# Kernel optimization log

Hardware: AMD Instinct MI355X
Metric: run time of the kernel (lower is better)

## Reference

```python
import jax, jax.numpy as jnp
import numpy as np

B, S, H, R = 2, 4096, 2048, 2048
NB, CW = 16, 4
BW = R // NB


def _block_diag_linear(x, w, b):
    # x: [B,S,R]; w: [NB,BW,BW]; b: [NB,BW]
    xb = x.reshape(x.shape[0], x.shape[1], NB, BW)
    out = jnp.einsum('bsni,nij->bsnj', xb, w) + b
    return out.reshape(x.shape)


def _causal_conv1d(x, conv_w, conv_b):
    # depthwise causal temporal conv: out[t] = sum_i w[i]*x[t-CW+1+i] + b
    xp = jnp.pad(x, ((0, 0), (CW - 1, 0), (0, 0)))
    out = conv_b
    for i in range(CW):
        out = out + conv_w[i] * xp[:, i:i + x.shape[1], :]
    return out


def _rg_lru_scan(x, x_gate_pre, a_gate_pre, a_param):
    gate_x = jax.nn.sigmoid(x_gate_pre)
    gate_a = jax.nn.sigmoid(a_gate_pre)
    log_a = -8.0 * gate_a * jax.nn.softplus(a_param)  # [B,S,R]
    a = jnp.exp(log_a)
    multiplier = jnp.sqrt(-jnp.expm1(2.0 * log_a))  # sqrt(1 - a^2)
    norm_x = x * gate_x * multiplier
    # h_t = a_t * h_{t-1} + norm_x_t via parallel associative scan over time
    def combine(c1, c2):
        a1, b1 = c1
        a2, b2 = c2
        return a1 * a2, a2 * b1 + b2
    _, h = jax.lax.associative_scan(combine, (a, norm_x), axis=1)
    return h


def setup_inputs() -> dict:
    key = jax.random.key(0)
    ks = jax.random.split(key, 9)
    x = jax.random.normal(ks[0], (B, S, H), dtype=jnp.float32)
    W_xy = jax.random.normal(ks[1], (2 * R, H), dtype=jnp.float32) / np.sqrt(H)
    ig_w = jax.random.normal(ks[2], (NB, BW, BW), dtype=jnp.float32) / np.sqrt(BW)
    ig_b = jnp.zeros((NB, BW), dtype=jnp.float32)
    ag_w = jax.random.normal(ks[3], (NB, BW, BW), dtype=jnp.float32) / np.sqrt(BW)
    ag_b = jnp.zeros((NB, BW), dtype=jnp.float32)
    # forget_init: a = a_real in [0.9, 0.999]; a_param = softplus^{-1}(-log(a_real))
    unif = jax.random.uniform(ks[4], (R,), dtype=jnp.float32)
    a_real = 0.5 * jnp.log(unif * (0.999 ** 2 - 0.9 ** 2) + 0.9 ** 2 + 1e-8)
    a_param = jnp.log(jnp.expm1(-a_real))
    conv_w = jax.random.normal(ks[5], (CW, R), dtype=jnp.float32) / np.sqrt(CW * R)
    conv_b = jnp.zeros((R,), dtype=jnp.float32)
    # resid_proj is zero-init in the module; use small random so output is non-trivial
    W_resid = 0.02 * jax.random.normal(ks[6], (H, R), dtype=jnp.float32)
    return {"x": x, "W_xy": W_xy, "ig_w": ig_w, "ig_b": ig_b,
            "ag_w": ag_w, "ag_b": ag_b, "a_param": a_param,
            "conv_w": conv_w, "conv_b": conv_b, "W_resid": W_resid}


def reference(x, W_xy, ig_w, ig_b, ag_w, ag_b, a_param, conv_w, conv_b, W_resid):
    xy = jnp.einsum('bsh,rh->bsr', x, W_xy)  # [B,S,2R]
    xr, y = jnp.split(xy, 2, axis=-1)
    xc = _causal_conv1d(xr, conv_w, conv_b)
    x_gate_pre = _block_diag_linear(xc, ig_w, ig_b)
    a_gate_pre = _block_diag_linear(xc, ag_w, ag_b)
    h = _rg_lru_scan(xc, x_gate_pre, a_gate_pre, a_param)
    out = jnp.einsum('bsr,hr->bsh', jax.nn.gelu(y, approximate=False) * h, W_resid)
    return out
```

## Files before the change

kernel.cpp:

```cpp
#include <hip/hip_runtime.h>
#include <hip/hip_bf16.h>

typedef __hip_bfloat16 bf16;
typedef __attribute__((ext_vector_type(8))) short s16x8;
typedef __attribute__((ext_vector_type(4))) float f32x4;

#define B_ 2
#define S_ 4096
#define H_ 2048
#define R_ 2048
#define M_ 8192
#define NB_ 16
#define BW_ 128
#define CHUNK 64
#define NCH 64

__device__ __forceinline__ short f2b_s(float f) {
    return (short)__builtin_bit_cast(unsigned short, __float2bfloat16(f));
}
__device__ __forceinline__ float b2f_s(short s) {
    unsigned int u = ((unsigned int)(unsigned short)s) << 16;
    return __builtin_bit_cast(float, u);
}
__device__ __forceinline__ float sigm_fast(float x) { return 1.f / (1.f + __expf(-x)); }

__device__ __forceinline__ void async_g2l(const void* g, void* l) {
    __builtin_amdgcn_global_load_lds((const __attribute__((address_space(1))) void*)g,
                                     (__attribute__((address_space(3))) void*)l, 16, 0, 0);
}

__global__ __launch_bounds__(256) void cast_all(const float* __restrict__ x,
                                                const float* __restrict__ wxy,
                                                const float* __restrict__ wres,
                                                bf16* __restrict__ xbf,
                                                bf16* __restrict__ wxyb,
                                                bf16* __restrict__ wresb) {
    int idx = blockIdx.x * 256 + threadIdx.x;
    const float* in; bf16* out; int off;
    if (idx < 2097152)      { in = x;    out = xbf;   off = idx; }
    else if (idx < 3145728) { in = wxy;  out = wxyb;  off = idx - 2097152; }
    else                    { in = wres; out = wresb; off = idx - 3145728; }
    size_t i8 = (size_t)off * 8;
    float4 v0 = *(const float4*)(in + i8);
    float4 v1 = *(const float4*)(in + i8 + 4);
    s16x8 o;
    o[0] = f2b_s(v0.x); o[1] = f2b_s(v0.y); o[2] = f2b_s(v0.z); o[3] = f2b_s(v0.w);
    o[4] = f2b_s(v1.x); o[5] = f2b_s(v1.y); o[6] = f2b_s(v1.z); o[7] = f2b_s(v1.w);
    *(s16x8*)(out + i8) = o;
}

__global__ __launch_bounds__(256) void wcast_T(const float* __restrict__ igw,
                                               const float* __restrict__ agw,
                                               const float* __restrict__ apar,
                                               bf16* __restrict__ wT,
                                               float* __restrict__ sp8) {
    int blk = blockIdx.x;
    int tid = threadIdx.x;
    if (blk == 32) {
#pragma unroll
        for (int it = 0; it < 8; ++it) {
            int r = it * 256 + tid;
            float ap = apar[r];
            sp8[r] = 8.f * (ap > 20.f ? ap : log1pf(expf(ap)));
        }
        return;
    }
    __shared__ float tile[128 * 129];
    int p = blk >> 4, n = blk & 15;
    const float* w = (p ? agw : igw) + (size_t)n * 16384;
#pragma unroll
    for (int it = 0; it < 64; ++it) {
        int u = it * 256 + tid;
        tile[(u >> 7) * 129 + (u & 127)] = w[u];
    }
    __syncthreads();
    bf16* o = wT + (size_t)blk * 16384;
#pragma unroll
    for (int it = 0; it < 64; ++it) {
        int u = it * 256 + tid;
        o[u] = __float2bfloat16(tile[(u & 127) * 129 + (u >> 7)]);
    }
}

__device__ __forceinline__ void store_c(float* p, float v) { *p = v; }
__device__ __forceinline__ void store_c(bf16* p, float v) { *p = __float2bfloat16(v); }

template <typename OutT>
__global__ __launch_bounds__(256, 4) void gemm_bt(const bf16* __restrict__ A,
                                                  const bf16* __restrict__ Bm,
                                                  OutT* __restrict__ C,
                                                  int K, int lda, int ldb, int ldc) {
    __shared__ __align__(16) short As[128 * 64];
    __shared__ __align__(16) short Bs[128 * 64];
    const int tid = threadIdx.x;
    const int lane = tid & 63, wave = tid >> 6;
    const int waveM = wave >> 1, waveN = wave & 1;
    const int mBase = blockIdx.y * 128, nBase = blockIdx.x * 128;
    const int fm = lane & 15, q = lane >> 4;

    f32x4 acc[4][4];
#pragma unroll
    for (int i = 0; i < 4; ++i)
#pragma unroll
        for (int j = 0; j < 4; ++j) acc[i][j] = (f32x4){0.f, 0.f, 0.f, 0.f};

    for (int k0 = 0; k0 < K; k0 += 64) {
        __syncthreads();
#pragma unroll
        for (int it = 0; it < 4; ++it) {
            int off = it * 4096 + tid * 16;
            int r = off >> 7;
            int g = ((off & 127) >> 4) ^ (r & 7);
            async_g2l(A + (size_t)(mBase + r) * lda + k0 + g * 8, (char*)As + off);
            async_g2l(Bm + (size_t)(nBase + r) * ldb + k0 + g * 8, (char*)Bs + off);
        }
        __syncthreads();
#pragma unroll
        for (int s = 0; s < 2; ++s) {
            s16x8 af[4], bfr[4];
#pragma unroll
            for (int i = 0; i < 4; ++i) {
                int row = waveM * 64 + i * 16 + fm;
                af[i] = *(const s16x8*)((char*)As + row * 128 + ((((s << 2) + q) ^ (row & 7)) << 4));
                int col = waveN * 64 + i * 16 + fm;
                bfr[i] = *(const s16x8*)((char*)Bs + col * 128 + ((((s << 2) + q) ^ (col & 7)) << 4));
            }
#pragma unroll
            for (int i = 0; i < 4; ++i)
#pragma unroll
                for (int j = 0; j < 4; ++j)
                    acc[i][j] = __builtin_amdgcn_mfma_f32_16x16x32_bf16(af[i], bfr[j], acc[i][j], 0, 0, 0);
        }
    }
#pragma unroll
    for (int i = 0; i < 4; ++i) {
        int rowg = mBase + waveM * 64 + i * 16 + q * 4;
#pragma unroll
        for (int j = 0; j < 4; ++j) {
            int colg = nBase + waveN * 64 + j * 16 + fm;
#pragma unroll
            for (int rr = 0; rr < 4; ++rr)
                store_c(C + (size_t)(rowg + rr) * ldc + colg, acc[i][j][rr]);
        }
    }
}

__global__ __launch_bounds__(256) void gate_kernel(const bf16* __restrict__ xy,
                                                   const float* __restrict__ cw,
                                                   const float* __restrict__ cb,
                                                   const bf16* __restrict__ wT,
                                                   const float* __restrict__ igb,
                                                   const float* __restrict__ agb,
                                                   const float* __restrict__ sp8,
                                                   bf16* __restrict__ hloc_out,
                                                   bf16* __restrict__ cum_out,
                                                   float* __restrict__ Ach,
                                                   float* __restrict__ Hla) {
    __shared__ __align__(16) short As[64 * 128];
    __shared__ __align__(16) char  Wmem[128 * 256];
    short* Xs   = (short*)Wmem;
    short* Ws   = (short*)Wmem;
    float* a_sh = (float*)Wmem;
    const int n = blockIdx.x;
    const int mBase = blockIdx.y * 64;
    const int tid = threadIdx.x;
    const int lane = tid & 63, wave = tid >> 6;
    const int fm = lane & 15, q = lane >> 4;
    const int t0 = mBase & (S_ - 1);

#pragma unroll
    for (int it = 0; it < 5; ++it) {
        int u = it * 256 + tid;
        if (u < 67 * 16) {
            int rr = u >> 4, gg = u & 15;
            s16x8 v = (s16x8){0, 0, 0, 0, 0, 0, 0, 0};
            if (t0 != 0 || rr >= 3) {
                int m = mBase + rr - 3;
                v = *(const s16x8*)(xy + (size_t)m * 4096 + n * BW_ + gg * 8);
            }
            *(s16x8*)((char*)Xs + u * 16) = v;
        }
    }
    __syncthreads();

    {
        int col = tid & 127, rh = tid >> 7;
        int rbase = n * BW_ + col;
        float w0c = cw[rbase], w1c = cw[R_ + rbase], w2c = cw[2 * R_ + rbase],
              w3c = cw[3 * R_ + rbase];
        float bc = cb[rbase];
        int r0 = rh * 32;
        float xm3 = b2f_s(Xs[(r0 + 0) * 128 + col]);
        float xm2 = b2f_s(Xs[(r0 + 1) * 128 + col]);
        float xm1 = b2f_s(Xs[(r0 + 2) * 128 + col]);
#pragma unroll
        for (int rw = 0; rw < 32; ++rw) {
            int row = r0 + rw;
            float x0 = b2f_s(Xs[(row + 3) * 128 + col]);
            float v = bc + w0c * xm3 + w1c * xm2 + w2c * xm1 + w3c * x0;
            xm3 = xm2; xm2 = xm1; xm1 = x0;
            *(short*)((char*)As + row * 256 + ((((col >> 3)) ^ (row & 15)) << 4) +
                      (col & 7) * 2) = f2b_s(v);
        }
    }
    __syncthreads();

    const bf16* w0 = wT + (size_t)n * 16384;
#pragma unroll
    for (int it = 0; it < 8; ++it) {
        int off = it * 4096 + tid * 16;
        int j = off >> 8;
        int g = ((off & 255) >> 4) ^ (j & 15);
        async_g2l(w0 + j * 128 + g * 8, (char*)Ws + off);
    }
    __syncthreads();

    f32x4 accI[8], accA[8];
#pragma unroll
    for (int jj = 0; jj < 8; ++jj) {
        accI[jj] = (f32x4){0.f, 0.f, 0.f, 0.f};
        accA[jj] = (f32x4){0.f, 0.f, 0.f, 0.f};
    }

    const int row = wave * 16 + fm;
#pragma unroll
    for (int s = 0; s < 4; ++s) {
        s16x8 af = *(const s16x8*)((char*)As + row * 256 + ((((s << 2) + q) ^ (row & 15)) << 4));
#pragma unroll
        for (int jj = 0; jj < 8; ++jj) {
            int wrow = jj * 16 + fm;
            s16x8 bw = *(const s16x8*)((char*)Ws + wrow * 256 + ((((s << 2) + q) ^ (wrow & 15)) << 4));
            accI[jj] = __builtin_amdgcn_mfma_f32_16x16x32_bf16(af, bw, accI[jj], 0, 0, 0);
        }
    }
    __syncthreads();
    const bf16* w1 = wT + (size_t)(NB_ + n) * 16384;
#pragma unroll
    for (int it = 0; it < 8; ++it) {
        int off = it * 4096 + tid * 16;
        int j = off >> 8;
        int g = ((off & 255) >> 4) ^ (j & 15);
        async_g2l(w1 + j * 128 + g * 8, (char*)Ws + off);
    }
    __syncthreads();
#pragma unroll
    for (int s = 0; s < 4; ++s) {
        s16x8 af = *(const s16x8*)((char*)As + row * 256 + ((((s << 2) + q) ^ (row & 15)) << 4));
#pragma unroll
        for (int jj = 0; jj < 8; ++jj) {
            int wrow = jj * 16 + fm;
            s16x8 bw = *(const s16x8*)((char*)Ws + wrow * 256 + ((((s << 2) + q) ^ (wrow & 15)) << 4));
            accA[jj] = __builtin_amdgcn_mfma_f32_16x16x32_bf16(af, bw, accA[jj], 0, 0, 0);
        }
    }
    __syncthreads();

#pragma unroll
    for (int jj = 0; jj < 8; ++jj) {
        int col = jj * 16 + fm;
        int r = n * BW_ + col;
        float bi = igb[r], ba = agb[r];
        float s8 = sp8[r];
#pragma unroll
        for (int rr = 0; rr < 4; ++rr) {
            int rowl = wave * 16 + q * 4 + rr;
            short* slot = (short*)((char*)As + rowl * 256 +
                          ((((col >> 3)) ^ (rowl & 15)) << 4) + (col & 7) * 2);
            float xcv = b2f_s(*slot);
            float xg = accI[jj][rr] + bi;
            float ag = accA[jj][rr] + ba;
            float la = -s8 * sigm_fast(ag);
            float av = __expf(la);
            float t2 = 2.f * la;
            float nem = (t2 > -0.125f)
                ? -t2 * (1.f + t2 * (0.5f + t2 * (0.16666667f + t2 * 0.04166667f)))
                : 1.f - av * av;
            float nxv = xcv * sigm_fast(xg) * sqrtf(nem);
            short nxs = f2b_s(nxv);
            a_sh[rowl * 128 + col] = av;
            *slot = nxs;
        }
    }
    __syncthreads();

    if (tid < 128) {
        int col = tid;
        float h = 0.f, cum = 1.f;
#pragma unroll 4
        for (int t = 0; t < CHUNK; ++t) {
            short* slot = (short*)((char*)As + t * 256 +
                          ((((col >> 3)) ^ (t & 15)) << 4) + (col & 7) * 2);
            float a = a_sh[t * 128 + col];
            float nxv = b2f_s(*slot);
            h = fmaf(a, h, nxv);
            cum *= a;
            *slot = f2b_s(h);
            a_sh[t * 128 + col] = cum;
        }
        int b = mBase >> 12, c = (mBase & (S_ - 1)) >> 6;
        int so = ((b * NCH + c) << 11) + n * BW_ + col;
        Ach[so] = cum;
        Hla[so] = h;
    }
    __syncthreads();

#pragma unroll
    for (int it = 0; it < 4; ++it) {
        int u = it * 256 + tid;
        int t = u >> 4, gg = u & 15;
        s16x8 hv = *(const s16x8*)((char*)As + t * 256 + ((gg ^ (t & 15)) << 4));
        s16x8 cv;
#pragma unroll
        for (int i = 0; i < 8; ++i) cv[i] = f2b_s(a_sh[t * 128 + gg * 8 + i]);
        size_t o = (size_t)(mBase + t) * R_ + n * BW_ + gg * 8;
        *(s16x8*)(hloc_out + o) = hv;
        *(s16x8*)(cum_out + o) = cv;
    }
}

__global__ __launch_bounds__(256) void scan_carry(const float* __restrict__ Ach,
                                                  const float* __restrict__ Hla,
                                                  float* __restrict__ carry) {
    int idx = blockIdx.x * 256 + threadIdx.x;
    int r = idx & (R_ - 1), b = idx >> 11;
    float cy = 0.f;
#pragma unroll 4
    for (int c = 0; c < NCH; ++c) {
        int o = (b * NCH + c) * R_ + r;
        carry[o] = cy;
        cy = fmaf(Ach[o], cy, Hla[o]);
    }
}

__global__ __launch_bounds__(256) void scan_passB(const bf16* __restrict__ hloc,
                                                  const bf16* __restrict__ cum,
                                                  const float* __restrict__ carry,
                                                  const bf16* __restrict__ xy,
                                                  bf16* __restrict__ g_out) {
    int idx = blockIdx.x * 256 + threadIdx.x;
    int m = idx >> 8;
    int r = (idx & 255) << 3;
    int b = m >> 12, c = (m & 4095) >> 6;
    int so = ((b * NCH + c) << 11) + r;
    size_t o = (size_t)m * R_ + r;
    s16x8 hv = *(const s16x8*)(hloc + o);
    s16x8 cv = *(const s16x8*)(cum + o);
    float4 cy0 = *(const float4*)(carry + so);
    float4 cy1 = *(const float4*)(carry + so + 4);
    s16x8 yv = *(const s16x8*)(xy + (size_t)m * 4096 + 2048 + r);
    float cya0 = cy0.x, cya1 = cy0.y, cya2 = cy0.z, cya3 = cy0.w;
    float cya4 = cy1.x, cya5 = cy1.y, cya6 = cy1.z, cya7 = cy1.w;
    s16x8 g;
#pragma unroll 8
    for (int i = 0; i < 8; ++i) {
        float cy = (i == 0) ? cya0 : (i == 1) ? cya1 : (i == 2) ? cya2 : (i == 3) ? cya3
                 : (i == 4) ? cya4 : (i == 5) ? cya5 : (i == 6) ? cya6 : cya7;
        float h = fmaf(b2f_s(cv[i]), cy, b2f_s(hv[i]));
        float y = b2f_s(yv[i]);
        float gg = 0.5f * y * (1.f + erff(y * 0.70710678f));
        g[i] = f2b_s(gg * h);
    }
    *(s16x8*)(g_out + o) = g;
}

extern "C" void kernel_launch(void* const* d_in, const int* in_sizes, int n_in,
                              void* d_out, int out_size, void* d_ws, size_t ws_size,
                              hipStream_t stream) {
    const float* x    = (const float*)d_in[0];
    const float* Wxy  = (const float*)d_in[1];
    const float* igw  = (const float*)d_in[2];
    const float* igb  = (const float*)d_in[3];
    const float* agw  = (const float*)d_in[4];
    const float* agb  = (const float*)d_in[5];
    const float* apar = (const float*)d_in[6];
    const float* cw   = (const float*)d_in[7];
    const float* cb   = (const float*)d_in[8];
    const float* Wres = (const float*)d_in[9];
    float* out = (float*)d_out;

    char* ws = (char*)d_ws;
    const size_t MiB = (size_t)1 << 20;
    bf16*  xbf   = (bf16*)(ws);
    bf16*  hloc  = (bf16*)(ws);
    bf16*  wxyb  = (bf16*)(ws + 32 * MiB);
    bf16*  wT    = (bf16*)(ws + 32 * MiB);
    float* sp8   = (float*)(ws + 33 * MiB + 65536);
    bf16*  xy    = (bf16*)(ws + 48 * MiB);
    bf16*  wresb = (bf16*)(ws + 112 * MiB);
    bf16*  g     = (bf16*)(ws + 120 * MiB);
    bf16*  cum   = (bf16*)(ws + 152 * MiB);
    float* Ach   = (float*)(ws + 184 * MiB);
    float* Hla   = (float*)(ws + 185 * MiB);
    float* cyb   = (float*)(ws + 186 * MiB);

    cast_all<<<14336, 256, 0, stream>>>(x, Wxy, Wres, xbf, wxyb, wresb);

    gemm_bt<bf16><<<dim3(32, 64), 256, 0, stream>>>(xbf, wxyb, xy, 2048, 2048, 2048, 4096);

    wcast_T<<<33, 256, 0, stream>>>(igw, agw, apar, wT, sp8);

    gate_kernel<<<dim3(NB_, 128), 256, 0, stream>>>(xy, cw, cb, wT, igb, agb, sp8,
                                                    hloc, cum, Ach, Hla);

    scan_carry<<<16, 256, 0, stream>>>(Ach, Hla, cyb);
    scan_passB<<<8192, 256, 0, stream>>>(hloc, cum, cyb, xy, g);

    gemm_bt<float><<<dim3(16, 64), 256, 0, stream>>>(g, wresb, out, 2048, 2048, 2048, 2048);
}
```

Baseline: 463.2 us.

## Fuse GELU into xy GEMM epilogue, pack scan carry inputs, split GEMM by batch

Moves the exact-erf GELU on the y half of the projection into the first GEMM's epilogue, so scan_passB only multiplies the already-activated y by h. Ach and Hla are packed into one float2 array, and scan_carry now loads eight chunks ahead before running its serial recurrence, which exposes more memory-level parallelism. The first GEMM is split into two launches, one per batch half, and cyb is relocated in the workspace. GELU is now applied to the fp32 accumulator before the bf16 rounding rather than after, which shifts numerics slightly, and the second launch adds a little launch overhead.

```diff
diff --git a/kernel.cpp b/kernel.cpp
--- a/kernel.cpp
+++ b/kernel.cpp
@@ -89,7 +89,8 @@
 __global__ __launch_bounds__(256, 4) void gemm_bt(const bf16* __restrict__ A,
                                                   const bf16* __restrict__ Bm,
                                                   OutT* __restrict__ C,
-                                                  int K, int lda, int ldb, int ldc) {
+                                                  int K, int lda, int ldb, int ldc,
+                                                  int gelu_from) {
     __shared__ __align__(16) short As[128 * 64];
     __shared__ __align__(16) short Bs[128 * 64];
     const int tid = threadIdx.x;
@@ -97,6 +98,7 @@
     const int waveM = wave >> 1, waveN = wave & 1;
     const int mBase = blockIdx.y * 128, nBase = blockIdx.x * 128;
     const int fm = lane & 15, q = lane >> 4;
+    const bool dog = (nBase >= gelu_from);
 
     f32x4 acc[4][4];
 #pragma unroll
@@ -139,8 +141,11 @@
         for (int j = 0; j < 4; ++j) {
             int colg = nBase + waveN * 64 + j * 16 + fm;
 #pragma unroll
-            for (int rr = 0; rr < 4; ++rr)
-                store_c(C + (size_t)(rowg + rr) * ldc + colg, acc[i][j][rr]);
+            for (int rr = 0; rr < 4; ++rr) {
+                float v = acc[i][j][rr];
+                if (dog) v = 0.5f * v * (1.f + erff(v * 0.70710678f));
+                store_c(C + (size_t)(rowg + rr) * ldc + colg, v);
+            }
         }
     }
 }
@@ -154,8 +159,7 @@
                                                    const float* __restrict__ sp8,
                                                    bf16* __restrict__ hloc_out,
                                                    bf16* __restrict__ cum_out,
-                                                   float* __restrict__ Ach,
-                                                   float* __restrict__ Hla) {
+                                                   float2* __restrict__ AH) {
     __shared__ __align__(16) short As[64 * 128];
     __shared__ __align__(16) char  Wmem[128 * 256];
     short* Xs   = (short*)Wmem;
@@ -299,8 +303,7 @@
         }
         int b = mBase >> 12, c = (mBase & (S_ - 1)) >> 6;
         int so = ((b * NCH + c) << 11) + n * BW_ + col;
-        Ach[so] = cum;
-        Hla[so] = h;
+        AH[so] = make_float2(cum, h);
     }
     __syncthreads();
 
@@ -318,17 +321,21 @@
     }
 }
 
-__global__ __launch_bounds__(256) void scan_carry(const float* __restrict__ Ach,
-                                                  const float* __restrict__ Hla,
+__global__ __launch_bounds__(256) void scan_carry(const float2* __restrict__ AH,
                                                   float* __restrict__ carry) {
     int idx = blockIdx.x * 256 + threadIdx.x;
     int r = idx & (R_ - 1), b = idx >> 11;
+    int base = b * NCH * R_ + r;
     float cy = 0.f;
-#pragma unroll 4
-    for (int c = 0; c < NCH; ++c) {
-        int o = (b * NCH + c) * R_ + r;
-        carry[o] = cy;
-        cy = fmaf(Ach[o], cy, Hla[o]);
+    for (int c0 = 0; c0 < NCH; c0 += 8) {
+        float2 v[8];
+#pragma unroll
+        for (int j = 0; j < 8; ++j) v[j] = AH[base + (c0 + j) * R_];
+#pragma unroll
+        for (int j = 0; j < 8; ++j) {
+            carry[base + (c0 + j) * R_] = cy;
+            cy = fmaf(v[j].x, cy, v[j].y);
+        }
     }
 }
 
@@ -356,9 +363,7 @@
         float cy = (i == 0) ? cya0 : (i == 1) ? cya1 : (i == 2) ? cya2 : (i == 3) ? cya3
                  : (i == 4) ? cya4 : (i == 5) ? cya5 : (i == 6) ? cya6 : cya7;
         float h = fmaf(b2f_s(cv[i]), cy, b2f_s(hv[i]));
-        float y = b2f_s(yv[i]);
-        float gg = 0.5f * y * (1.f + erff(y * 0.70710678f));
-        g[i] = f2b_s(gg * h);
+        g[i] = f2b_s(b2f_s(yv[i]) * h);
     }
     *(s16x8*)(g_out + o) = g;
 }
@@ -385,25 +390,29 @@
     bf16*  wxyb  = (bf16*)(ws + 32 * MiB);
     bf16*  wT    = (bf16*)(ws + 32 * MiB);
     float* sp8   = (float*)(ws + 33 * MiB + 65536);
+    float* cyb   = (float*)(ws + 36 * MiB);
     bf16*  xy    = (bf16*)(ws + 48 * MiB);
     bf16*  wresb = (bf16*)(ws + 112 * MiB);
     bf16*  g     = (bf16*)(ws + 120 * MiB);
     bf16*  cum   = (bf16*)(ws + 152 * MiB);
-    float* Ach   = (float*)(ws + 184 * MiB);
-    float* Hla   = (float*)(ws + 185 * MiB);
-    float* cyb   = (float*)(ws + 186 * MiB);
+    float2* AH   = (float2*)(ws + 184 * MiB);
 
     cast_all<<<14336, 256, 0, stream>>>(x, Wxy, Wres, xbf, wxyb, wresb);
 
-    gemm_bt<bf16><<<dim3(32, 64), 256, 0, stream>>>(xbf, wxyb, xy, 2048, 2048, 2048, 4096);
+    gemm_bt<bf16><<<dim3(32, 32), 256, 0, stream>>>(xbf, wxyb, xy,
+                                                    2048, 2048, 2048, 4096, 2048);
+    gemm_bt<bf16><<<dim3(32, 32), 256, 0, stream>>>(xbf + (size_t)4096 * 2048, wxyb,
+                                                    xy + (size_t)4096 * 4096,
+                                                    2048, 2048, 2048, 4096, 2048);
 
     wcast_T<<<33, 256, 0, stream>>>(igw, agw, apar, wT, sp8);
 
     gate_kernel<<<dim3(NB_, 128), 256, 0, stream>>>(xy, cw, cb, wT, igb, agb, sp8,
-                                                    hloc, cum, Ach, Hla);
-
-    scan_carry<<<16, 256, 0, stream>>>(Ach, Hla, cyb);
+                                                    hloc, cum, AH);
+
+    scan_carry<<<16, 256, 0, stream>>>(AH, cyb);
     scan_passB<<<8192, 256, 0, stream>>>(hloc, cum, cyb, xy, g);
 
-    gemm_bt<float><<<dim3(16, 64), 256, 0, stream>>>(g, wresb, out, 2048, 2048, 2048, 2048);
-}
+    gemm_bt<float><<<dim3(16, 64), 256, 0, stream>>>(g, wresb, out,
+                                                     2048, 2048, 2048, 2048, 1 << 30);
+}
```

After: 478.6 us. 1.03x slower.
